# Performance work log

Measured on AMD Instinct MI355X. Metric: run time of the kernel, lower is better.

The kernel has to match this reference:

```python
import jax, jax.numpy as jnp
import numpy as np

N, E, K, F, R = 100000, 200000, 16, 32, 2
EPS = 1e-5

def setup_inputs() -> dict:
    key = jax.random.key(0)
    ks = jax.random.split(key, 32)
    inp = {}
    inp['x'] = jax.random.normal(ks[0], (N, F), jnp.float32)
    inp['y'] = jax.random.normal(ks[1], (E, F), jnp.float32)
    inp['deg_g'] = jax.random.uniform(ks[2], (N, 1), jnp.float32)
    inp['deg_lg'] = jax.random.uniform(ks[3], (E, 1), jnp.float32)
    inp['t_g'] = jax.random.randint(ks[4], (N, K), 0, N)
    inp['tt_g'] = jax.random.randint(ks[5], (N, K), 0, N)
    inp['t_lg'] = jax.random.randint(ks[6], (E, K), 0, E)
    inp['tt_lg'] = jax.random.randint(ks[7], (E, K), 0, E)
    inp['dst'] = jax.random.randint(ks[8], (E,), 0, N)
    inp['pm_pd'] = jax.random.randint(ks[9], (E,), 0, N)
    i = [10]
    def mk(shape):
        a = jax.random.normal(ks[i[0]], shape, jnp.float32) * 0.1
        i[0] += 1
        return a
    for nm in ['theta_x', 'theta_deg', 'theta_y', 'gamma_y', 'gamma_deg', 'gamma_x']:
        inp[nm + '_w'] = mk((F, F)); inp[nm + '_b'] = mk((F,))
    inp['theta_r_w'] = mk((R, F, F)); inp['theta_r_b'] = mk((R, F))
    inp['gamma_r_w'] = mk((R, F, F)); inp['gamma_r_b'] = mk((R, F))
    inp['bn_x_w'] = jnp.ones((F,), jnp.float32); inp['bn_x_b'] = jnp.zeros((F,), jnp.float32)
    inp['bn_y_w'] = jnp.ones((F,), jnp.float32); inp['bn_y_b'] = jnp.zeros((F,), jnp.float32)
    return inp

def _lin(a, w, b):
    return a @ w + b

def _bn(a, w, b):
    # BatchNorm1d in training mode: biased batch stats
    m = a.mean(axis=0)
    v = a.var(axis=0)
    return (a - m) / jnp.sqrt(v + EPS) * w + b

def _aggregate(z, t, tt):
    # per-node gather+sum over neighbor index lists (t: radius-0, tt: radius-1)
    return jnp.stack([z[t].sum(axis=1), z[tt].sum(axis=1)])  # [R, M, F]

def reference(x, y, deg_g, deg_lg, t_g, tt_g, t_lg, tt_lg, dst, pm_pd,
              theta_x_w, theta_x_b, theta_deg_w, theta_deg_b, theta_y_w, theta_y_b,
              gamma_y_w, gamma_y_b, gamma_deg_w, gamma_deg_b, gamma_x_w, gamma_x_b,
              theta_r_w, theta_r_b, gamma_r_w, gamma_r_b,
              bn_x_w, bn_x_b, bn_y_w, bn_y_b):
    n = F // 2
    pmpd_x = x[pm_pd]                                   # [E, F] embedding gather
    zs = _aggregate(x, t_g, tt_g)                        # [R, N, F]
    sum_x = jnp.einsum('rnf,rfo->no', zs, theta_r_w) + theta_r_b.sum(axis=0)
    pmpd_y = jax.ops.segment_sum(y, dst, num_segments=x.shape[0])  # copy_edge + sum
    xo = (_lin(x, theta_x_w, theta_x_b)
          + _lin(deg_g * x, theta_deg_w, theta_deg_b)
          + sum_x
          + _lin(pmpd_y, theta_y_w, theta_y_b))
    xo = jnp.concatenate([xo[:, :n], jax.nn.relu(xo[:, n:])], axis=1)
    xo = _bn(xo, bn_x_w, bn_x_b)
    zy = _aggregate(y, t_lg, tt_lg)                      # [R, E, F]
    sum_y = jnp.einsum('ref,rfo->eo', zy, gamma_r_w) + gamma_r_b.sum(axis=0)
    yo = (_lin(y, gamma_y_w, gamma_y_b)
          + _lin(deg_lg * y, gamma_deg_w, gamma_deg_b)
          + sum_y
          + _lin(pmpd_x, gamma_x_w, gamma_x_b))
    yo = jnp.concatenate([yo[:, :n], jax.nn.relu(yo[:, n:])], axis=1)
    yo = _bn(yo, bn_y_w, bn_y_b)
    return xo, yo
```

## Files before the change

kernel.cpp:

```cpp
#include <hip/hip_runtime.h>

#define NN 100000
#define NE 200000
#define MT (NN + NE)

typedef unsigned short u16;
typedef unsigned int u32;
typedef __attribute__((ext_vector_type(8))) short bf16x8;
typedef __attribute__((ext_vector_type(4))) float f32x4;

__device__ __forceinline__ float bf2f(u16 u) {
    union { u32 i; float f; } v; v.i = ((u32)u) << 16; return v.f;
}
__device__ __forceinline__ u16 f2bf(float f) {
    union { u32 i; float f; } v; v.f = f;
    u32 r = v.i + 0x7fffu + ((v.i >> 16) & 1u);
    return (u16)(r >> 16);
}
__device__ __forceinline__ void unpack2(u32 u, float& lo, float& hi) {
    union { u32 i; float f; } a, b;
    a.i = u << 16; b.i = u & 0xffff0000u;
    lo = a.f; hi = b.f;
}
__device__ __forceinline__ u32 pack2(float a, float b) {
    return (u32)f2bf(a) | ((u32)f2bf(b) << 16);
}
__device__ __forceinline__ float loadf(const void* p, size_t i, int f32) {
    return f32 ? ((const float*)p)[i] : bf2f(((const u16*)p)[i]);
}

__global__ void detect_kernel(const u32* __restrict__ x, int* flag) {
    __shared__ int cnt;
    if (threadIdx.x == 0) cnt = 0;
    __syncthreads();
    int bad = 0;
    for (int i = threadIdx.x; i < 1024; i += 256) {
        u32 e = (x[i] >> 7) & 0xFF;
        if (e == 0xFF || (e > 0 && (e < 107 || e > 134))) bad++;
    }
    atomicAdd(&cnt, bad);
    __syncthreads();
    if (threadIdx.x == 0) *flag = (cnt > 256) ? 1 : 0;
}

__global__ __launch_bounds__(256) void prep_kernel(
    const void* txw, const void* tdw, const void* tyw,
    const void* gyw, const void* gdw, const void* gxw,
    const void* trw, const void* grw,
    const void* txb, const void* tdb, const void* tyb,
    const void* gyb, const void* gdb, const void* gxb,
    const void* trb, const void* grb,
    u16* Bfx, u16* Bfy, float* bx, float* by, const int* flagp)
{
    int f32 = *flagp;
    int t = blockIdx.x * 256 + threadIdx.x;
    if (t < 10240) {
        int side = t / 5120;
        int e = t - side * 5120;
        int b = e >> 9, lane = (e >> 3) & 63, j = e & 7;
        int m = b >> 1;
        int k = ((lane >> 4) << 3) + j;
        int f = ((lane & 15) << 1) | (b & 1);
        size_t idx = (size_t)k * 32 + f;
        float v;
        if (side == 0) {
            v = (m == 0) ? loadf(txw, idx, f32) : (m == 1) ? loadf(tdw, idx, f32)
              : (m == 2) ? loadf(trw, idx, f32) : (m == 3) ? loadf(trw, 1024 + idx, f32)
              : loadf(gxw, idx, f32);
            Bfx[e] = f2bf(v);
        } else {
            v = (m == 0) ? loadf(gyw, idx, f32) : (m == 1) ? loadf(gdw, idx, f32)
              : (m == 2) ? loadf(grw, idx, f32) : (m == 3) ? loadf(grw, 1024 + idx, f32)
              : loadf(tyw, idx, f32);
            Bfy[e] = f2bf(v);
        }
    } else if (t < 10304) {
        int f = t - 10240;
        if (f < 32) {
            bx[f] = loadf(txb, f, f32) + loadf(tdb, f, f32) + loadf(tyb, f, f32)
                  + loadf(trb, f, f32) + loadf(trb, 32 + f, f32);
        } else {
            f -= 32;
            by[f] = loadf(gyb, f, f32) + loadf(gdb, f, f32) + loadf(gxb, f, f32)
                  + loadf(grb, f, f32) + loadf(grb, 32 + f, f32);
        }
    }
}

__global__ __launch_bounds__(256, 4) void gemm_side(
    const void* __restrict__ feat, const u16* __restrict__ Bf,
    const float* __restrict__ bias, const void* __restrict__ deg,
    u16* __restrict__ Self, u16* __restrict__ T,
    u16* __restrict__ TT,   u16* __restrict__ Aux,
    int nwaves, const int* __restrict__ flagp)
{
    __shared__ __align__(16) u16 sbuf[4][4][512];
    int f32 = *flagp;
    int lane = threadIdx.x & 63;
    int wib  = threadIdx.x >> 6;
    int wid = blockIdx.x * 4 + wib;
    if (wid >= nwaves) return;
    int r0 = wid * 16;

    union { u16 s[8]; bf16x8 v; } au;
    {
        size_t eoff = (size_t)(r0 + (lane & 15)) * 32 + ((lane >> 4) << 3);
        if (f32) {
            const float4* fp = (const float4*)((const float*)feat + eoff);
            float4 A0 = fp[0], A1 = fp[1];
            au.s[0] = f2bf(A0.x); au.s[1] = f2bf(A0.y);
            au.s[2] = f2bf(A0.z); au.s[3] = f2bf(A0.w);
            au.s[4] = f2bf(A1.x); au.s[5] = f2bf(A1.y);
            au.s[6] = f2bf(A1.z); au.s[7] = f2bf(A1.w);
        } else {
            au.v = *(const bf16x8*)((const u16*)feat + eoff);
        }
    }
    f32x4 acc[10];
    const u16* bp = Bf + lane * 8;
#pragma unroll
    for (int b = 0; b < 10; ++b) {
        bf16x8 bfr = *(const bf16x8*)(bp + b * 512);
        f32x4 z = {0.f, 0.f, 0.f, 0.f};
        acc[b] = __builtin_amdgcn_mfma_f32_16x16x32_bf16(au.v, bfr, z, 0, 0, 0);
    }

    int n = lane & 15, quad = lane >> 4;
    int rowb = r0 + quad * 4;
    float bev = bias[2 * n], bov = bias[2 * n + 1];

#pragma unroll
    for (int i = 0; i < 4; ++i) {
        float dgi = loadf(deg, rowb + i, f32);
        int rr = (quad * 4 + i) * 32 + 2 * n;
        *(u32*)&sbuf[wib][0][rr] = pack2(acc[0][i] + dgi * acc[2][i] + bev,
                                         acc[1][i] + dgi * acc[3][i] + bov);
        *(u32*)&sbuf[wib][1][rr] = pack2(acc[4][i], acc[5][i]);
        *(u32*)&sbuf[wib][2][rr] = pack2(acc[6][i], acc[7][i]);
        *(u32*)&sbuf[wib][3][rr] = pack2(acc[8][i], acc[9][i]);
    }
    __asm__ volatile("s_waitcnt lgkmcnt(0)" ::: "memory");

    int lr = lane >> 2, ch = (lane & 3) * 8;
    int lo = lr * 32 + ch;
    size_t go = (size_t)(r0 + lr) * 32 + ch;
    *(uint4*)(Self + go) = *(const uint4*)&sbuf[wib][0][lo];
    *(uint4*)(T   + go)  = *(const uint4*)&sbuf[wib][1][lo];
    *(uint4*)(TT  + go)  = *(const uint4*)&sbuf[wib][2][lo];
    *(uint4*)(Aux + go)  = *(const uint4*)&sbuf[wib][3][lo];
}

__global__ __launch_bounds__(256) void scatter_y(
    const u16* __restrict__ Yaux, const int* __restrict__ dst,
    float* __restrict__ xacc)
{
    int tid = blockIdx.x * 256 + threadIdx.x;
    if (tid >= NE * 16) return;
    int e = tid >> 4, p = tid & 15;
    int d = dst[e];
    u32 pair = *(const u32*)(Yaux + (size_t)e * 32 + 2 * p);
    float lo, hi;
    unpack2(pair, lo, hi);
    float* px = xacc + (size_t)d * 32 + 2 * p;
    atomicAdd(px, lo);
    atomicAdd(px + 1, hi);
}

__global__ __launch_bounds__(256) void gather_fused(
    const u16* __restrict__ Xself, const u16* __restrict__ Xt,
    const u16* __restrict__ Xtt,   const u16* __restrict__ Xaux,
    const u16* __restrict__ Yself, const u16* __restrict__ Yt,
    const u16* __restrict__ Ytt,
    const float* __restrict__ xacc,
    const int* __restrict__ t_g, const int* __restrict__ tt_g,
    const int* __restrict__ t_lg, const int* __restrict__ tt_lg,
    const int* __restrict__ pm_pd,
    u16* __restrict__ pre_h,
    float* __restrict__ stats)
{
    __shared__ int s_t[1024];
    __shared__ int s_tt[1024];
    __shared__ float s_sum[32];
    __shared__ float s_sq[32];
    bool is_y = (blockIdx.x >= 1563);
    int M = is_y ? NE : NN;
    const u16 *Self, *T, *TT;
    const int *tl, *ttl;
    if (is_y) { Self = Yself; T = Yt; TT = Ytt; tl = t_lg; ttl = tt_lg; }
    else      { Self = Xself; T = Xt; TT = Xtt; tl = t_g;  ttl = tt_g; }
    float* ss = stats + (is_y ? 64 : 0);

    if (threadIdx.x < 32) { s_sum[threadIdx.x] = 0.f; s_sq[threadIdx.x] = 0.f; }
    int row0 = (is_y ? (int)blockIdx.x - 1563 : (int)blockIdx.x) * 64;
    int lim = (M - row0) * 16;
    for (int i = threadIdx.x; i < 1024; i += 256) {
        s_t[i]  = (i < lim) ? tl[row0 * 16 + i]  : 0;
        s_tt[i] = (i < lim) ? ttl[row0 * 16 + i] : 0;
    }
    __syncthreads();

    int lr = threadIdx.x >> 2, q = threadIdx.x & 3;
    int r = row0 + lr;
    bool act = r < M;
    int rc = act ? r : row0;

    float a[8];
    {
        uint4 u = *(const uint4*)(Self + (size_t)rc * 32 + q * 8);
        unpack2(u.x, a[0], a[1]); unpack2(u.y, a[2], a[3]);
        unpack2(u.z, a[4], a[5]); unpack2(u.w, a[6], a[7]);
    }
    const int* il  = &s_t[lr * 16];
    const int* ill = &s_tt[lr * 16];
#pragma unroll
    for (int batch = 0; batch < 2; ++batch) {
        uint4 g[8];
#pragma unroll
        for (int j = 0; j < 8; ++j)
            g[j] = *(const uint4*)(T + (size_t)il[batch * 8 + j] * 32 + q * 8);
#pragma unroll
        for (int j = 0; j < 8; ++j) {
            float e0, e1, e2, e3, e4, e5, e6, e7;
            unpack2(g[j].x, e0, e1); unpack2(g[j].y, e2, e3);
            unpack2(g[j].z, e4, e5); unpack2(g[j].w, e6, e7);
            a[0] += e0; a[1] += e1; a[2] += e2; a[3] += e3;
            a[4] += e4; a[5] += e5; a[6] += e6; a[7] += e7;
        }
    }
#pragma unroll
    for (int batch = 0; batch < 2; ++batch) {
        uint4 g[8];
#pragma unroll
        for (int j = 0; j < 8; ++j)
            g[j] = *(const uint4*)(TT + (size_t)ill[batch * 8 + j] * 32 + q * 8);
#pragma unroll
        for (int j = 0; j < 8; ++j) {
            float e0, e1, e2, e3, e4, e5, e6, e7;
            unpack2(g[j].x, e0, e1); unpack2(g[j].y, e2, e3);
            unpack2(g[j].z, e4, e5); unpack2(g[j].w, e6, e7);
            a[0] += e0; a[1] += e1; a[2] += e2; a[3] += e3;
            a[4] += e4; a[5] += e5; a[6] += e6; a[7] += e7;
        }
    }
    if (!is_y) {
        float4 b0 = *(const float4*)(xacc + (size_t)rc * 32 + q * 8);
        float4 b1 = *(const float4*)(xacc + (size_t)rc * 32 + q * 8 + 4);
        a[0] += b0.x; a[1] += b0.y; a[2] += b0.z; a[3] += b0.w;
        a[4] += b1.x; a[5] += b1.y; a[6] += b1.z; a[7] += b1.w;
    } else {
        int ai = pm_pd[rc];
        uint4 g = *(const uint4*)(Xaux + (size_t)ai * 32 + q * 8);
        float e0, e1, e2, e3, e4, e5, e6, e7;
        unpack2(g.x, e0, e1); unpack2(g.y, e2, e3);
        unpack2(g.z, e4, e5); unpack2(g.w, e6, e7);
        a[0] += e0; a[1] += e1; a[2] += e2; a[3] += e3;
        a[4] += e4; a[5] += e5; a[6] += e6; a[7] += e7;
    }
    if (q >= 2) {
#pragma unroll
        for (int i = 0; i < 8; ++i) a[i] = fmaxf(a[i], 0.f);
    }
    if (act) {
        size_t orow = (size_t)(is_y ? NN + r : r) * 32 + q * 8;
        uint4 o;
        o.x = pack2(a[0], a[1]); o.y = pack2(a[2], a[3]);
        o.z = pack2(a[4], a[5]); o.w = pack2(a[6], a[7]);
        *(uint4*)(pre_h + orow) = o;
    } else {
#pragma unroll
        for (int i = 0; i < 8; ++i) a[i] = 0.f;
    }
#pragma unroll
    for (int i = 0; i < 8; ++i) {
        atomicAdd(&s_sum[q * 8 + i], a[i]);
        atomicAdd(&s_sq[q * 8 + i], a[i] * a[i]);
    }
    __syncthreads();
    if (threadIdx.x < 32) {
        atomicAdd(&ss[threadIdx.x], s_sum[threadIdx.x]);
        atomicAdd(&ss[32 + threadIdx.x], s_sq[threadIdx.x]);
    }
}

__global__ void finalize_stats(
    const float* stats,
    const void* bnxw, const void* bnxb, const void* bnyw, const void* bnyb,
    float* scsh, const int* flagp)
{
    int f32 = *flagp;
    int f = threadIdx.x;
    if (f < 32) {
        float m = stats[f] / (float)NN;
        float var = stats[32 + f] / (float)NN - m * m;
        float inv = rsqrtf(var + 1e-5f);
        float sc = loadf(bnxw, f, f32) * inv;
        scsh[f] = sc; scsh[32 + f] = loadf(bnxb, f, f32) - m * sc;
    } else if (f < 64) {
        int g = f - 32;
        float m = stats[64 + g] / (float)NE;
        float var = stats[96 + g] / (float)NE - m * m;
        float inv = rsqrtf(var + 1e-5f);
        float sc = loadf(bnyw, g, f32) * inv;
        scsh[64 + g] = sc; scsh[96 + g] = loadf(bnyb, g, f32) - m * sc;
    }
}

__global__ __launch_bounds__(256) void apply_bn(
    const u16* __restrict__ pre_h, const float* __restrict__ scsh,
    void* __restrict__ out, const int* __restrict__ flagp)
{
    int f32 = *flagp;
    int tid = blockIdx.x * 256 + threadIdx.x;
    if (tid >= MT * 8) return;
    int fq = (tid & 7) * 4;
    const float* sc = (tid < NN * 8) ? scsh : scsh + 64;
    ushort4 u = ((const ushort4*)pre_h)[tid];
    float o0 = bf2f(u.x) * sc[fq + 0] + sc[32 + fq + 0];
    float o1 = bf2f(u.y) * sc[fq + 1] + sc[32 + fq + 1];
    float o2 = bf2f(u.z) * sc[fq + 2] + sc[32 + fq + 2];
    float o3 = bf2f(u.w) * sc[fq + 3] + sc[32 + fq + 3];
    if (f32) {
        float4 o; o.x = o0; o.y = o1; o.z = o2; o.w = o3;
        ((float4*)out)[tid] = o;
    } else {
        ushort4 o; o.x = f2bf(o0); o.y = f2bf(o1); o.z = f2bf(o2); o.w = f2bf(o3);
        ((ushort4*)out)[tid] = o;
    }
}

extern "C" void kernel_launch(void* const* d_in, const int* in_sizes, int n_in,
                              void* d_out, int out_size, void* d_ws, size_t ws_size,
                              hipStream_t stream)
{
    const void* x      = d_in[0];
    const void* y      = d_in[1];
    const void* deg_g  = d_in[2];
    const void* deg_lg = d_in[3];
    const int* t_g   = (const int*)d_in[4];
    const int* tt_g  = (const int*)d_in[5];
    const int* t_lg  = (const int*)d_in[6];
    const int* tt_lg = (const int*)d_in[7];
    const int* dst   = (const int*)d_in[8];
    const int* pm_pd = (const int*)d_in[9];

    char* ws = (char*)d_ws;
    int*   flag = (int*)ws;
    u16* Bfx   = (u16*)(ws + 256);
    u16* Bfy   = Bfx + 5120;
    float* bx  = (float*)(ws + 24576);
    float* by  = bx + 32;
    float* stats = by + 32;
    float* scsh  = stats + 128;
    u16* Xself = (u16*)(ws + 65536);
    u16* Xt    = Xself + (size_t)NN * 32;
    u16* Xtt   = Xt    + (size_t)NN * 32;
    u16* Xaux  = Xtt   + (size_t)NN * 32;
    u16* Yself = Xaux  + (size_t)NN * 32;
    u16* Yt    = Yself + (size_t)NE * 32;
    u16* Ytt   = Yt    + (size_t)NE * 32;
    u16* Yaux  = Ytt   + (size_t)NE * 32;
    float* xacc = (float*)(Yaux + (size_t)NE * 32);
    u16* pre_h = (u16*)(xacc + (size_t)NN * 32);

    hipMemsetAsync(stats, 0, 256 * sizeof(float), stream);
    hipMemsetAsync(xacc, 0, (size_t)NN * 32 * sizeof(float), stream);

    detect_kernel<<<1, 256, 0, stream>>>((const u32*)x, flag);
    prep_kernel<<<41, 256, 0, stream>>>(
        d_in[10], d_in[12], d_in[14], d_in[16], d_in[18], d_in[20],
        d_in[22], d_in[24],
        d_in[11], d_in[13], d_in[15], d_in[17], d_in[19], d_in[21],
        d_in[23], d_in[25],
        Bfx, Bfy, bx, by, flag);
    gemm_side<<<1563, 256, 0, stream>>>(x, Bfx, bx, deg_g,
                                        Xself, Xt, Xtt, Xaux, 6250, flag);
    gemm_side<<<3125, 256, 0, stream>>>(y, Bfy, by, deg_lg,
                                        Yself, Yt, Ytt, Yaux, 12500, flag);
    scatter_y<<<12500, 256, 0, stream>>>(Yaux, dst, xacc);
    gather_fused<<<4688, 256, 0, stream>>>(Xself, Xt, Xtt, Xaux, Yself, Yt, Ytt,
                                           xacc, t_g, tt_g, t_lg, tt_lg, pm_pd,
                                           pre_h, stats);
    finalize_stats<<<1, 64, 0, stream>>>(stats, d_in[26], d_in[27], d_in[28],
                                         d_in[29], scsh, flag);
    apply_bn<<<9375, 256, 0, stream>>>(pre_h, scsh, d_out, flag);
}
```

Before: 444.7 us.

## Replace per-feature atomic scatter with bucketed edge lists gathered in fused kernel

Swaps the per-feature float atomicAdd scatter of Yaux into xacc for a per-destination edge list of fixed capacity, built with one atomic per edge. The fused gather kernel then sums the listed edges' Yaux rows directly, and only overflow edges beyond the capacity fall back to atomics. This is meant to remove the 6.4M float atomics, at the cost of an extra memset, an index list, a data-dependent loop inside the gather kernel, and the loss of a fixed summation order for the edge contributions.

```diff
diff --git a/kernel.cpp b/kernel.cpp
--- a/kernel.cpp
+++ b/kernel.cpp
@@ -3,6 +3,7 @@
 #define NN 100000
 #define NE 200000
 #define MT (NN + NE)
+#define ECAP 16
 
 typedef unsigned short u16;
 typedef unsigned int u32;
@@ -150,28 +151,31 @@
     *(uint4*)(Aux + go)  = *(const uint4*)&sbuf[wib][3][lo];
 }
 
-__global__ __launch_bounds__(256) void scatter_y(
-    const u16* __restrict__ Yaux, const int* __restrict__ dst,
+__global__ __launch_bounds__(256) void fill_edges(
+    const int* __restrict__ dst, int* __restrict__ cnt,
+    int* __restrict__ elist, const u16* __restrict__ Yaux,
     float* __restrict__ xacc)
 {
-    int tid = blockIdx.x * 256 + threadIdx.x;
-    if (tid >= NE * 16) return;
-    int e = tid >> 4, p = tid & 15;
+    int e = blockIdx.x * 256 + threadIdx.x;
+    if (e >= NE) return;
     int d = dst[e];
-    u32 pair = *(const u32*)(Yaux + (size_t)e * 32 + 2 * p);
-    float lo, hi;
-    unpack2(pair, lo, hi);
-    float* px = xacc + (size_t)d * 32 + 2 * p;
-    atomicAdd(px, lo);
-    atomicAdd(px + 1, hi);
+    int pos = atomicAdd(&cnt[d], 1);
+    if (pos < ECAP) {
+        elist[(size_t)d * ECAP + pos] = e;
+    } else {
+        const u16* yr = Yaux + (size_t)e * 32;
+        float* px = xacc + (size_t)d * 32;
+        for (int f = 0; f < 32; ++f) atomicAdd(px + f, bf2f(yr[f]));
+    }
 }
 
 __global__ __launch_bounds__(256) void gather_fused(
     const u16* __restrict__ Xself, const u16* __restrict__ Xt,
     const u16* __restrict__ Xtt,   const u16* __restrict__ Xaux,
     const u16* __restrict__ Yself, const u16* __restrict__ Yt,
-    const u16* __restrict__ Ytt,
+    const u16* __restrict__ Ytt,   const u16* __restrict__ Yaux,
     const float* __restrict__ xacc,
+    const int* __restrict__ cnt,   const int* __restrict__ elist,
     const int* __restrict__ t_g, const int* __restrict__ tt_g,
     const int* __restrict__ t_lg, const int* __restrict__ tt_lg,
     const int* __restrict__ pm_pd,
@@ -243,6 +247,18 @@
         }
     }
     if (!is_y) {
+        int c = cnt[rc];
+        if (c > ECAP) c = ECAP;
+        const int* el = elist + (size_t)rc * ECAP;
+        for (int k = 0; k < c; ++k) {
+            int e = el[k];
+            uint4 g = *(const uint4*)(Yaux + (size_t)e * 32 + q * 8);
+            float e0, e1, e2, e3, e4, e5, e6, e7;
+            unpack2(g.x, e0, e1); unpack2(g.y, e2, e3);
+            unpack2(g.z, e4, e5); unpack2(g.w, e6, e7);
+            a[0] += e0; a[1] += e1; a[2] += e2; a[3] += e3;
+            a[4] += e4; a[5] += e5; a[6] += e6; a[7] += e7;
+        }
         float4 b0 = *(const float4*)(xacc + (size_t)rc * 32 + q * 8);
         float4 b1 = *(const float4*)(xacc + (size_t)rc * 32 + q * 8 + 4);
         a[0] += b0.x; a[1] += b0.y; a[2] += b0.z; a[3] += b0.w;
@@ -361,9 +377,12 @@
     u16* Yaux  = Ytt   + (size_t)NE * 32;
     float* xacc = (float*)(Yaux + (size_t)NE * 32);
     u16* pre_h = (u16*)(xacc + (size_t)NN * 32);
+    int* cnt   = (int*)(pre_h + (size_t)MT * 32);
+    int* elist = cnt + NN;
 
     hipMemsetAsync(stats, 0, 256 * sizeof(float), stream);
     hipMemsetAsync(xacc, 0, (size_t)NN * 32 * sizeof(float), stream);
+    hipMemsetAsync(cnt, 0, (size_t)NN * sizeof(int), stream);
 
     detect_kernel<<<1, 256, 0, stream>>>((const u32*)x, flag);
     prep_kernel<<<41, 256, 0, stream>>>(
@@ -376,9 +395,11 @@
                                         Xself, Xt, Xtt, Xaux, 6250, flag);
     gemm_side<<<3125, 256, 0, stream>>>(y, Bfy, by, deg_lg,
                                         Yself, Yt, Ytt, Yaux, 12500, flag);
-    scatter_y<<<12500, 256, 0, stream>>>(Yaux, dst, xacc);
-    gather_fused<<<4688, 256, 0, stream>>>(Xself, Xt, Xtt, Xaux, Yself, Yt, Ytt,
-                                           xacc, t_g, tt_g, t_lg, tt_lg, pm_pd,
+    fill_edges<<<782, 256, 0, stream>>>(dst, cnt, elist, Yaux, xacc);
+    gather_fused<<<4688, 256, 0, stream>>>(Xself, Xt, Xtt, Xaux,
+                                           Yself, Yt, Ytt, Yaux,
+                                           xacc, cnt, elist,
+                                           t_g, tt_g, t_lg, tt_lg, pm_pd,
                                            pre_h, stats);
     finalize_stats<<<1, 64, 0, stream>>>(stats, d_in[26], d_in[27], d_in[28],
                                          d_in[29], scsh, flag);
```

After: 433.6 us. 1.03x faster.
